# Performance work log

Measured on AMD Instinct MI355X. Metric: run time of the kernel, lower is better.

The kernel has to match this reference:

```python
import jax, jax.numpy as jnp
import numpy as np

B, T, H = 32, 1024, 1024


def setup_inputs() -> dict:
    key = jax.random.key(0)
    k1, k2, k3, k4, k5 = jax.random.split(key, 5)
    h_t = jax.random.normal(k1, (B, H), dtype=jnp.float32)
    enc_out = jax.random.normal(k2, (B, T, H), dtype=jnp.float32)
    src_mask = jnp.ones((B, T), dtype=bool)
    s = 1.0 / np.sqrt(H)
    Wa = jax.random.normal(k3, (H, H), dtype=jnp.float32) * s
    Ua = jax.random.normal(k4, (H, H), dtype=jnp.float32) * s
    va = jax.random.normal(k5, (H,), dtype=jnp.float32) * s
    return {"h_t": h_t, "enc_out": enc_out, "src_mask": src_mask,
            "Wa": Wa, "Ua": Ua, "va": va}


def reference(h_t, enc_out, src_mask, Wa, Ua, va):
    # h_proj: [B,H] ; enc_proj: [B,T,H]
    h_proj = h_t @ Wa.T
    enc_proj = jnp.einsum('bth,kh->btk', enc_out, Ua)
    # additive score: va . tanh(Wa h + Ua enc)  -> [B,T]
    e = jnp.einsum('bth,h->bt', jnp.tanh(h_proj[:, None, :] + enc_proj), va)
    e = jnp.where(src_mask, e, -jnp.inf)
    attn = jax.nn.softmax(e, axis=1)                     # [B,T]
    context = jnp.einsum('bt,bth->bh', attn, enc_out)    # [B,H]
    return context, attn
```

## Files before the change

kernel.cpp:

```cpp
#include <hip/hip_runtime.h>

#define BB 32
#define TT 1024
#define HH 1024
#define MM (BB * TT)

typedef __bf16 bf16x8 __attribute__((ext_vector_type(8)));
typedef float  f32x4  __attribute__((ext_vector_type(4)));

__device__ __forceinline__ void async_copy16(const void* g, void* l) {
  __builtin_amdgcn_global_load_lds(
      (const __attribute__((address_space(1))) void*)g,
      (__attribute__((address_space(3))) void*)l, 16, 0, 0);
}

__device__ __forceinline__ float fast_tanh(float x) {
  float e2 = __expf(2.f * x);
  return 1.f - 2.f * __builtin_amdgcn_rcpf(e2 + 1.f);
}

#define NCHUNK_ENC 4194304
#define CVT_BLKS   2112
#define CVT_STRIDE (CVT_BLKS * 256)
__global__ __launch_bounds__(256) void prep_kernel(
    const float* __restrict__ enc, const float* __restrict__ Ua,
    const float* __restrict__ h_t, const float* __restrict__ Wa,
    __bf16* __restrict__ encb, __bf16* __restrict__ uab,
    float* __restrict__ hp, float* __restrict__ e) {
  const int blk = blockIdx.x;
  const int tid = threadIdx.x;

  if (blk < CVT_BLKS) {
    int F = blk * 256 + tid;
#pragma unroll
    for (int it = 0; it < 8; ++it, F += CVT_STRIDE) {
      const float* src;
      __bf16* dst;
      int R;
      if (F < NCHUNK_ENC) { src = enc; dst = encb; R = F; }
      else                { src = Ua;  dst = uab;  R = F - NCHUNK_ENC; }
      const int c   = R & 2047;
      const int t   = R >> 11;
      const int kt  = t & 15;
      const int rt  = t >> 4;
      const int u   = c >> 10;
      const int idx = (c >> 3) & 127;
      const int s   = c & 7;
      const int g   = s ^ (idx & 7);
      const int row = (idx & 63) + ((idx >> 6) & 1) * 128 + u * 64;
      const float* sp = src + (((size_t)rt * 256 + row) << 10) + (kt << 6) + (g << 3);
      f32x4 a  = *(const f32x4*)sp;
      f32x4 b2 = *(const f32x4*)(sp + 4);
      bf16x8 o;
      o[0] = (__bf16)a[0];  o[1] = (__bf16)a[1];
      o[2] = (__bf16)a[2];  o[3] = (__bf16)a[3];
      o[4] = (__bf16)b2[0]; o[5] = (__bf16)b2[1];
      o[6] = (__bf16)b2[2]; o[7] = (__bf16)b2[3];
      *(bf16x8*)(dst + (size_t)R * 8) = o;
    }
  } else if (blk < 2240) {
    const int hb = blk - CVT_BLKS;
    const int b  = hb >> 2;
    const int k  = (hb & 3) * 256 + tid;
    __shared__ float hs[HH];
    for (int i = tid; i < HH; i += 256) hs[i] = h_t[b * HH + i];
    __syncthreads();
    const float4* w  = (const float4*)(Wa + (size_t)k * HH);
    const float4* hv = (const float4*)hs;
    float acc = 0.f;
#pragma unroll 8
    for (int i = 0; i < HH / 4; ++i) {
      float4 a = w[i];
      float4 h = hv[i];
      acc += a.x * h.x + a.y * h.y + a.z * h.z + a.w * h.w;
    }
    hp[b * HH + k] = acc;
  } else {
    f32x4 z = {0.f, 0.f, 0.f, 0.f};
    f32x4* ep = (f32x4*)e;
#pragma unroll
    for (int i = 0; i < 32; ++i) ep[i * 256 + tid] = z;
  }
}

__global__ __launch_bounds__(128) void hproj_kernel(
    const float* __restrict__ h_t, const float* __restrict__ Wa,
    float* __restrict__ hp) {
  const int k = blockIdx.x * 128 + threadIdx.x;
  const int b = blockIdx.y;
  __shared__ float hs[HH];
  for (int i = threadIdx.x; i < HH; i += 128) hs[i] = h_t[b * HH + i];
  __syncthreads();
  const float4* w  = (const float4*)(Wa + (size_t)k * HH);
  const float4* hv = (const float4*)hs;
  float acc = 0.f;
#pragma unroll 8
  for (int i = 0; i < HH / 4; ++i) {
    float4 a = w[i];
    float4 h = hv[i];
    acc += a.x * h.x + a.y * h.y + a.z * h.z + a.w * h.w;
  }
  hp[b * HH + k] = acc;
}

__global__ __launch_bounds__(512, 2) void score_8ph_kernel(
    const __bf16* __restrict__ encb, const __bf16* __restrict__ uab,
    const float* __restrict__ hp, const float* __restrict__ va,
    float* __restrict__ e) {
  __shared__ __bf16 As[2][16384];
  __shared__ __bf16 Bs[2][16384];

  const int wg = blockIdx.x;
  const int sw = (wg & 7) * 64 + (wg >> 3);
  const int nt = sw & 3;
  const int mt = sw >> 2;
  const int b  = mt >> 2;

  const int tid  = threadIdx.x;
  const int lane = tid & 63;
  const int wid  = tid >> 6;
  const int wr   = wid >> 2;
  const int wc   = wid & 3;
  const int rl   = lane & 15;
  const int kq   = lane >> 4;
  const int e7   = rl & 7;

  const __bf16* Ag = encb + ((size_t)(mt * 16) << 14);
  const __bf16* Bg = uab  + ((size_t)(nt * 16) << 14);

  const int s0 = ((kq ^ e7) << 4);
  const int s1 = (((kq + 4) ^ e7) << 4);
  const int arow = (rl + wr * 64) * 128;
  const int brow = (rl + (wc >> 1) * 64) * 128 + (wc & 1) * 16384;

#define LDA(buf, mi, sl) (*(const bf16x8*)((const char*)(buf) + \
    (((mi) >> 2) * 16384 + ((mi) & 3) * 2048) + arow + (sl)))
#define LDB(buf, nj, sl) (*(const bf16x8*)((const char*)(buf) + \
    ((nj) * 2048) + brow + (sl)))

#define STAGE(gb, kt2, lp, u) do { \
    const __bf16* _g = (gb) + (((size_t)(kt2)) << 14) + (((u) << 10) + tid) * 8; \
    __bf16* _l = (lp) + (((u) << 10) + tid) * 8; \
    async_copy16(_g, _l); \
    async_copy16(_g + 4096, _l + 4096); \
  } while (0)

#define MFMA16(ml, kkb) do { \
    _Pragma("unroll") \
    for (int nj = 0; nj < 4; ++nj) { \
      acc[(ml) + 0][nj] = __builtin_amdgcn_mfma_f32_16x16x32_bf16(af0, bfr[(kkb) + nj], acc[(ml) + 0][nj], 0, 0, 0); \
      acc[(ml) + 1][nj] = __builtin_amdgcn_mfma_f32_16x16x32_bf16(af1, bfr[(kkb) + nj], acc[(ml) + 1][nj], 0, 0, 0); \
      acc[(ml) + 2][nj] = __builtin_amdgcn_mfma_f32_16x16x32_bf16(af2, bfr[(kkb) + nj], acc[(ml) + 2][nj], 0, 0, 0); \
      acc[(ml) + 3][nj] = __builtin_amdgcn_mfma_f32_16x16x32_bf16(af3, bfr[(kkb) + nj], acc[(ml) + 3][nj], 0, 0, 0); \
    } \
  } while (0)

  f32x4 acc[8][4] = {};
  bf16x8 bfr[8];

  STAGE(Ag, 0, &As[0][0], 0);
  STAGE(Bg, 0, &Bs[0][0], 0);
  STAGE(Bg, 0, &Bs[0][0], 1);
  STAGE(Ag, 0, &As[0][0], 1);
  STAGE(Bg, 1, &Bs[1][0], 0);
  STAGE(Bg, 1, &Bs[1][0], 1);
  STAGE(Ag, 1, &As[1][0], 0);
  asm volatile("s_waitcnt vmcnt(6)" ::: "memory");
  __builtin_amdgcn_s_barrier();

  for (int t = 0; t < 15; ++t) {
    const int p = t & 1;
    const char* Ab = (const char*)&As[p][0];
    const char* Bb = (const char*)&Bs[p][0];

    {
#pragma unroll
      for (int nj = 0; nj < 4; ++nj) { bfr[nj] = LDB(Bb, nj, s0); bfr[4 + nj] = LDB(Bb, nj, s1); }
      bf16x8 af0 = LDA(Ab, 0, s0), af1 = LDA(Ab, 1, s0), af2 = LDA(Ab, 2, s0), af3 = LDA(Ab, 3, s0);
      STAGE(Ag, t + 1, &As[p ^ 1][0], 1);
      __builtin_amdgcn_s_barrier();
      asm volatile("s_waitcnt lgkmcnt(0)" ::: "memory");
      __builtin_amdgcn_s_setprio(1);
      MFMA16(0, 0);
      __builtin_amdgcn_s_setprio(0);
      __builtin_amdgcn_s_barrier();
    }
    {
      bf16x8 af0 = LDA(Ab, 0, s1), af1 = LDA(Ab, 1, s1), af2 = LDA(Ab, 2, s1), af3 = LDA(Ab, 3, s1);
      if (t < 14) STAGE(Bg, t + 2, &Bs[p][0], 0);
      __builtin_amdgcn_s_barrier();
      asm volatile("s_waitcnt lgkmcnt(0)" ::: "memory");
      __builtin_amdgcn_s_setprio(1);
      MFMA16(0, 4);
      __builtin_amdgcn_s_setprio(0);
      __builtin_amdgcn_s_barrier();
    }
    {
      bf16x8 af0 = LDA(Ab, 4, s0), af1 = LDA(Ab, 5, s0), af2 = LDA(Ab, 6, s0), af3 = LDA(Ab, 7, s0);
      if (t < 14) STAGE(Bg, t + 2, &Bs[p][0], 1);
      __builtin_amdgcn_s_barrier();
      asm volatile("s_waitcnt lgkmcnt(0)" ::: "memory");
      __builtin_amdgcn_s_setprio(1);
      MFMA16(4, 0);
      __builtin_amdgcn_s_setprio(0);
      __builtin_amdgcn_s_barrier();
    }
    {
      bf16x8 af0 = LDA(Ab, 4, s1), af1 = LDA(Ab, 5, s1), af2 = LDA(Ab, 6, s1), af3 = LDA(Ab, 7, s1);
      if (t < 14) STAGE(Ag, t + 2, &As[p][0], 0);
      __builtin_amdgcn_s_barrier();
      asm volatile("s_waitcnt lgkmcnt(0)" ::: "memory");
      __builtin_amdgcn_s_setprio(1);
      MFMA16(4, 4);
      __builtin_amdgcn_s_setprio(0);
      if (t < 14) asm volatile("s_waitcnt vmcnt(6)" ::: "memory");
      else        asm volatile("s_waitcnt vmcnt(0)" ::: "memory");
      __builtin_amdgcn_s_barrier();
    }
  }

  {
    const char* Ab = (const char*)&As[1][0];
    const char* Bb = (const char*)&Bs[1][0];
    {
#pragma unroll
      for (int nj = 0; nj < 4; ++nj) { bfr[nj] = LDB(Bb, nj, s0); bfr[4 + nj] = LDB(Bb, nj, s1); }
      bf16x8 af0 = LDA(Ab, 0, s0), af1 = LDA(Ab, 1, s0), af2 = LDA(Ab, 2, s0), af3 = LDA(Ab, 3, s0);
      __builtin_amdgcn_s_barrier();
      asm volatile("s_waitcnt lgkmcnt(0)" ::: "memory");
      __builtin_amdgcn_s_setprio(1);
      MFMA16(0, 0);
      __builtin_amdgcn_s_setprio(0);
      __builtin_amdgcn_s_barrier();
    }
    {
      bf16x8 af0 = LDA(Ab, 0, s1), af1 = LDA(Ab, 1, s1), af2 = LDA(Ab, 2, s1), af3 = LDA(Ab, 3, s1);
      __builtin_amdgcn_s_barrier();
      asm volatile("s_waitcnt lgkmcnt(0)" ::: "memory");
      __builtin_amdgcn_s_setprio(1);
      MFMA16(0, 4);
      __builtin_amdgcn_s_setprio(0);
      __builtin_amdgcn_s_barrier();
    }
    {
      bf16x8 af0 = LDA(Ab, 4, s0), af1 = LDA(Ab, 5, s0), af2 = LDA(Ab, 6, s0), af3 = LDA(Ab, 7, s0);
      __builtin_amdgcn_s_barrier();
      asm volatile("s_waitcnt lgkmcnt(0)" ::: "memory");
      __builtin_amdgcn_s_setprio(1);
      MFMA16(4, 0);
      __builtin_amdgcn_s_setprio(0);
      __builtin_amdgcn_s_barrier();
    }
    {
      bf16x8 af0 = LDA(Ab, 4, s1), af1 = LDA(Ab, 5, s1), af2 = LDA(Ab, 6, s1), af3 = LDA(Ab, 7, s1);
      __builtin_amdgcn_s_barrier();
      asm volatile("s_waitcnt lgkmcnt(0)" ::: "memory");
      __builtin_amdgcn_s_setprio(1);
      MFMA16(4, 4);
      __builtin_amdgcn_s_setprio(0);
    }
  }

  const float* hpb = hp + (b << 10);
#pragma unroll
  for (int mi = 0; mi < 8; ++mi) {
    float rs[4] = {0.f, 0.f, 0.f, 0.f};
#pragma unroll
    for (int nj = 0; nj < 4; ++nj) {
      const int col  = nt * 256 + wc * 64 + nj * 16 + rl;
      const float hv = hpb[col];
      const float vv = va[col];
#pragma unroll
      for (int j = 0; j < 4; ++j)
        rs[j] += fast_tanh(acc[mi][nj][j] + hv) * vv;
    }
#pragma unroll
    for (int j = 0; j < 4; ++j) {
      float r = rs[j];
      r += __shfl_xor(r, 1);
      r += __shfl_xor(r, 2);
      r += __shfl_xor(r, 4);
      r += __shfl_xor(r, 8);
      if (rl == 0)
        atomicAdd(&e[mt * 256 + wr * 128 + mi * 16 + kq * 4 + j], r);
    }
  }
#undef LDA
#undef LDB
#undef STAGE
#undef MFMA16
}

#define BM 128
#define BN 128
#define BK 32

__device__ __forceinline__ bf16x8 cvt8(const float* p) {
  f32x4 a = *(const f32x4*)p;
  f32x4 b = *(const f32x4*)(p + 4);
  bf16x8 r;
  r[0] = (__bf16)a[0]; r[1] = (__bf16)a[1]; r[2] = (__bf16)a[2]; r[3] = (__bf16)a[3];
  r[4] = (__bf16)b[0]; r[5] = (__bf16)b[1]; r[6] = (__bf16)b[2]; r[7] = (__bf16)b[3];
  return r;
}

__device__ __forceinline__ void score_epilogue(
    f32x4 acc[4][4], int m0, int n0, int b, int lane, int wr, int wc,
    const float* __restrict__ hp, const float* __restrict__ va,
    float* __restrict__ e) {
  const int rl = lane & 15;
  const int rq = lane >> 4;
#pragma unroll
  for (int mi = 0; mi < 4; ++mi) {
    float rs[4] = {0.f, 0.f, 0.f, 0.f};
#pragma unroll
    for (int nj = 0; nj < 4; ++nj) {
      const int col  = n0 + wc * 64 + nj * 16 + rl;
      const float hv = hp[(b << 10) + col];
      const float vv = va[col];
#pragma unroll
      for (int j = 0; j < 4; ++j)
        rs[j] += fast_tanh(acc[mi][nj][j] + hv) * vv;
    }
#pragma unroll
    for (int j = 0; j < 4; ++j) {
      float r = rs[j];
      r += __shfl_xor(r, 1);
      r += __shfl_xor(r, 2);
      r += __shfl_xor(r, 4);
      r += __shfl_xor(r, 8);
      if (rl == 0)
        atomicAdd(&e[m0 + wr * 64 + mi * 16 + rq * 4 + j], r);
    }
  }
}

__global__ __launch_bounds__(256) void score_f32_kernel(
    const float* __restrict__ enc, const float* __restrict__ Ua,
    const float* __restrict__ hp, const float* __restrict__ va,
    float* __restrict__ e) {
  const int m0 = blockIdx.x * BM;
  const int n0 = blockIdx.y * BN;
  const int b  = m0 >> 10;

  __shared__ float As[BM * BK];
  __shared__ float Bs[BN * BK];

  const int tid  = threadIdx.x;
  const int lane = tid & 63;
  const int wid  = tid >> 6;
  const int wr   = wid >> 1;
  const int wc   = wid & 1;

  f32x4 acc[4][4] = {};

  const int srow = tid >> 3;
  const int scol = (tid & 7) * 4;
  const float* gA = enc + (((size_t)(m0 + srow)) << 10) + scol;
  const float* gB = Ua  + (((size_t)(n0 + srow)) << 10) + scol;
  float* lA = As + srow * BK + scol;
  float* lB = Bs + srow * BK + scol;

  for (int kt = 0; kt < HH / BK; ++kt) {
    const int h0 = kt * BK;
    __syncthreads();
#pragma unroll
    for (int i = 0; i < 4; ++i) {
      async_copy16(gA + ((size_t)(i * 32) << 10) + h0, lA + i * 32 * BK);
      async_copy16(gB + ((size_t)(i * 32) << 10) + h0, lB + i * 32 * BK);
    }
    __syncthreads();

    const int koff = (lane >> 4) * 8;
    const int rl   = lane & 15;
    bf16x8 af[4], bfr[4];
#pragma unroll
    for (int mi = 0; mi < 4; ++mi)
      af[mi] = cvt8(As + (wr * 64 + mi * 16 + rl) * BK + koff);
#pragma unroll
    for (int nj = 0; nj < 4; ++nj)
      bfr[nj] = cvt8(Bs + (wc * 64 + nj * 16 + rl) * BK + koff);
#pragma unroll
    for (int mi = 0; mi < 4; ++mi)
#pragma unroll
      for (int nj = 0; nj < 4; ++nj)
        acc[mi][nj] = __builtin_amdgcn_mfma_f32_16x16x32_bf16(
            af[mi], bfr[nj], acc[mi][nj], 0, 0, 0);
  }

  score_epilogue(acc, m0, n0, b, lane, wr, wc, hp, va, e);
}

__global__ __launch_bounds__(256) void softmax_kernel(
    const float* __restrict__ e, const int* __restrict__ mask,
    float* __restrict__ attn) {
  const int b   = blockIdx.x;
  const int tid = threadIdx.x;
  const float* eb = e + (b << 10);
  const int*   mb = mask + (b << 10);
  float v[4];
  float mx = -INFINITY;
#pragma unroll
  for (int j = 0; j < 4; ++j) {
    const int t = tid + j * 256;
    float x = mb[t] ? eb[t] : -INFINITY;
    v[j] = x;
    mx = fmaxf(mx, x);
  }
#pragma unroll
  for (int s = 1; s < 64; s <<= 1) mx = fmaxf(mx, __shfl_xor(mx, s));
  __shared__ float redm[4];
  if ((tid & 63) == 0) redm[tid >> 6] = mx;
  __syncthreads();
  mx = fmaxf(fmaxf(redm[0], redm[1]), fmaxf(redm[2], redm[3]));

  float s = 0.f;
#pragma unroll
  for (int j = 0; j < 4; ++j) { v[j] = __expf(v[j] - mx); s += v[j]; }
#pragma unroll
  for (int st = 1; st < 64; st <<= 1) s += __shfl_xor(s, st);
  __shared__ float reds[4];
  if ((tid & 63) == 0) reds[tid >> 6] = s;
  __syncthreads();
  s = reds[0] + reds[1] + reds[2] + reds[3];
  const float inv = 1.f / s;
#pragma unroll
  for (int j = 0; j < 4; ++j) attn[(b << 10) + tid + j * 256] = v[j] * inv;
}

__global__ __launch_bounds__(256) void context2_kernel(
    const __bf16* __restrict__ encb, const float* __restrict__ attn,
    float* __restrict__ ctx) {
  const int q   = blockIdx.x;
  const int b   = blockIdx.y;
  const int tid = threadIdx.x;
  const int h8l = tid & 15;
  const int tq  = tid >> 4;
  const int h8g = q * 16 + h8l;
  const int kt  = h8g >> 3;
  const int g   = h8g & 7;

  __shared__ float at[1024];
  for (int i = tid; i < 1024; i += 256) at[i] = attn[(b << 10) + i];
  __syncthreads();

  const int rt = b * 4 + (tq >> 2);
  const int u  = tq & 1;
  const int b7 = (tq >> 1) & 1;
  const __bf16* base = encb + (((size_t)(rt * 16 + kt)) << 14)
                       + (u << 13) + (b7 << 12);
  const float* ap = at + tq * 64;

  float acc[8] = {};
#pragma unroll 8
  for (int j = 0; j < 64; ++j) {
    bf16x8 v = *(const bf16x8*)(base + j * 64 + ((g ^ (j & 7)) << 3));
    const float w = ap[j];
#pragma unroll
    for (int ee = 0; ee < 8; ++ee) acc[ee] += w * (float)v[ee];
  }

  __shared__ float red[16][16][8];
#pragma unroll
  for (int ee = 0; ee < 8; ++ee) red[tq][h8l][ee] = acc[ee];
  __syncthreads();

  if (tid < 128) {
    const int h8 = tid >> 3;
    const int ee = tid & 7;
    float s = 0.f;
#pragma unroll
    for (int r = 0; r < 16; ++r) s += red[r][h8][ee];
    ctx[(b << 10) + q * 128 + h8 * 8 + ee] = s;
  }
}

__global__ __launch_bounds__(256) void context_kernel(
    const float* __restrict__ attn, const float* __restrict__ enc,
    float* __restrict__ ctx) {
  const int h  = blockIdx.x * 256 + threadIdx.x;
  const int b  = blockIdx.y;
  const int t0 = blockIdx.z * 128;
  const float* ab = attn + (b << 10) + t0;
  const float* eb = enc + (((size_t)(b << 10) + t0) << 10) + h;
  float acc = 0.f;
#pragma unroll 4
  for (int t = 0; t < 128; ++t)
    acc = fmaf(ab[t], eb[(size_t)t << 10], acc);
  atomicAdd(&ctx[(b << 10) + h], acc);
}

extern "C" void kernel_launch(void* const* d_in, const int* in_sizes, int n_in,
                              void* d_out, int out_size, void* d_ws, size_t ws_size,
                              hipStream_t stream) {
  const float* h_t  = (const float*)d_in[0];
  const float* enc  = (const float*)d_in[1];
  const int*   mask = (const int*)d_in[2];
  const float* Wa   = (const float*)d_in[3];
  const float* Ua   = (const float*)d_in[4];
  const float* va   = (const float*)d_in[5];

  float* out = (float*)d_out;
  float* e   = (float*)d_ws;
  float* hp  = e + MM;

  const size_t base   = 2 * (size_t)MM * sizeof(float);
  const size_t encb_n = (size_t)MM * HH;
  const size_t uab_n  = (size_t)HH * HH;
  const size_t need   = base + (encb_n + uab_n) * sizeof(__bf16);

  if (ws_size >= need) {
    __bf16* encb = (__bf16*)((char*)d_ws + base);
    __bf16* uab  = encb + encb_n;
    prep_kernel<<<2241, 256, 0, stream>>>(enc, Ua, h_t, Wa, encb, uab, hp, e);
    score_8ph_kernel<<<512, 512, 0, stream>>>(encb, uab, hp, va, e);
    softmax_kernel<<<BB, 256, 0, stream>>>(e, mask, out + BB * HH);
    context2_kernel<<<dim3(8, BB), 256, 0, stream>>>(encb, out + BB * HH, out);
  } else {
    hipMemsetAsync(e, 0, MM * sizeof(float), stream);
    hipMemsetAsync(out, 0, BB * HH * sizeof(float), stream);
    hproj_kernel<<<dim3(HH / 128, BB), 128, 0, stream>>>(h_t, Wa, hp);
    score_f32_kernel<<<dim3(MM / BM, HH / BN), 256, 0, stream>>>(enc, Ua, hp, va, e);
    softmax_kernel<<<BB, 256, 0, stream>>>(e, mask, out + BB * HH);
    context_kernel<<<dim3(HH / 256, BB, 8), 256, 0, stream>>>(out + BB * HH, enc, out);
  }
}
```

Before: 156.9 us.

## Fuse enc fp32-to-bf16 conversion into score GEMM A-tile loading

Drops the separate pass that converted the whole encoder tensor to a swizzled bf16 copy. The score kernel now loads fp32 A tiles from global into registers, converts them, and writes bf16 into shared memory inside the pipelined loop. Ua conversion moves into a small prep kernel, and the context kernel reads fp32 enc directly. This removes a 128MB read plus 64MB write round trip. In exchange the GEMM uses more registers (occupancy hint lowered to 1), does synchronous register-staged loads instead of async LDS copies, and the context pass reads twice the bytes.

```diff
diff --git a/kernel.cpp b/kernel.cpp
--- a/kernel.cpp
+++ b/kernel.cpp
@@ -19,49 +19,16 @@
   return 1.f - 2.f * __builtin_amdgcn_rcpf(e2 + 1.f);
 }
 
-#define NCHUNK_ENC 4194304
-#define CVT_BLKS   2112
-#define CVT_STRIDE (CVT_BLKS * 256)
-__global__ __launch_bounds__(256) void prep_kernel(
-    const float* __restrict__ enc, const float* __restrict__ Ua,
-    const float* __restrict__ h_t, const float* __restrict__ Wa,
-    __bf16* __restrict__ encb, __bf16* __restrict__ uab,
+__global__ __launch_bounds__(256) void mini_prep_kernel(
+    const float* __restrict__ Ua, const float* __restrict__ h_t,
+    const float* __restrict__ Wa, __bf16* __restrict__ uab,
     float* __restrict__ hp, float* __restrict__ e) {
   const int blk = blockIdx.x;
   const int tid = threadIdx.x;
 
-  if (blk < CVT_BLKS) {
-    int F = blk * 256 + tid;
-#pragma unroll
-    for (int it = 0; it < 8; ++it, F += CVT_STRIDE) {
-      const float* src;
-      __bf16* dst;
-      int R;
-      if (F < NCHUNK_ENC) { src = enc; dst = encb; R = F; }
-      else                { src = Ua;  dst = uab;  R = F - NCHUNK_ENC; }
-      const int c   = R & 2047;
-      const int t   = R >> 11;
-      const int kt  = t & 15;
-      const int rt  = t >> 4;
-      const int u   = c >> 10;
-      const int idx = (c >> 3) & 127;
-      const int s   = c & 7;
-      const int g   = s ^ (idx & 7);
-      const int row = (idx & 63) + ((idx >> 6) & 1) * 128 + u * 64;
-      const float* sp = src + (((size_t)rt * 256 + row) << 10) + (kt << 6) + (g << 3);
-      f32x4 a  = *(const f32x4*)sp;
-      f32x4 b2 = *(const f32x4*)(sp + 4);
-      bf16x8 o;
-      o[0] = (__bf16)a[0];  o[1] = (__bf16)a[1];
-      o[2] = (__bf16)a[2];  o[3] = (__bf16)a[3];
-      o[4] = (__bf16)b2[0]; o[5] = (__bf16)b2[1];
-      o[6] = (__bf16)b2[2]; o[7] = (__bf16)b2[3];
-      *(bf16x8*)(dst + (size_t)R * 8) = o;
-    }
-  } else if (blk < 2240) {
-    const int hb = blk - CVT_BLKS;
-    const int b  = hb >> 2;
-    const int k  = (hb & 3) * 256 + tid;
+  if (blk < 128) {
+    const int b = blk >> 2;
+    const int k = (blk & 3) * 256 + tid;
     __shared__ float hs[HH];
     for (int i = tid; i < HH; i += 256) hs[i] = h_t[b * HH + i];
     __syncthreads();
@@ -75,6 +42,29 @@
       acc += a.x * h.x + a.y * h.y + a.z * h.z + a.w * h.w;
     }
     hp[b * HH + k] = acc;
+  } else if (blk < 256) {
+    int F = (blk - 128) * 256 + tid;
+#pragma unroll
+    for (int it = 0; it < 4; ++it, F += 32768) {
+      const int c   = F & 2047;
+      const int t   = F >> 11;
+      const int kt  = t & 15;
+      const int rt  = t >> 4;
+      const int u   = c >> 10;
+      const int idx = (c >> 3) & 127;
+      const int s   = c & 7;
+      const int g   = s ^ (idx & 7);
+      const int row = (idx & 63) + ((idx >> 6) & 1) * 128 + u * 64;
+      const float* sp = Ua + (((size_t)rt * 256 + row) << 10) + (kt << 6) + (g << 3);
+      f32x4 a  = *(const f32x4*)sp;
+      f32x4 b2 = *(const f32x4*)(sp + 4);
+      bf16x8 o;
+      o[0] = (__bf16)a[0];  o[1] = (__bf16)a[1];
+      o[2] = (__bf16)a[2];  o[3] = (__bf16)a[3];
+      o[4] = (__bf16)b2[0]; o[5] = (__bf16)b2[1];
+      o[6] = (__bf16)b2[2]; o[7] = (__bf16)b2[3];
+      *(bf16x8*)(uab + (size_t)F * 8) = o;
+    }
   } else {
     f32x4 z = {0.f, 0.f, 0.f, 0.f};
     f32x4* ep = (f32x4*)e;
@@ -103,8 +93,8 @@
   hp[b * HH + k] = acc;
 }
 
-__global__ __launch_bounds__(512, 2) void score_8ph_kernel(
-    const __bf16* __restrict__ encb, const __bf16* __restrict__ uab,
+__global__ __launch_bounds__(512, 1) void score_8ph_kernel(
+    const float* __restrict__ enc, const __bf16* __restrict__ uab,
     const float* __restrict__ hp, const float* __restrict__ va,
     float* __restrict__ e) {
   __shared__ __bf16 As[2][16384];
@@ -125,8 +115,11 @@
   const int kq   = lane >> 4;
   const int e7   = rl & 7;
 
-  const __bf16* Ag = encb + ((size_t)(mt * 16) << 14);
-  const __bf16* Bg = uab  + ((size_t)(nt * 16) << 14);
+  const float* Af = enc + ((size_t)(mt * 256) << 10);
+  const __bf16* Bg = uab + ((size_t)(nt * 16) << 14);
+
+  const int aidx = tid >> 3;
+  const int ag8  = ((tid & 7) ^ (aidx & 7)) << 3;
 
   const int s0 = ((kq ^ e7) << 4);
   const int s1 = (((kq + 4) ^ e7) << 4);
@@ -138,11 +131,33 @@
 #define LDB(buf, nj, sl) (*(const bf16x8*)((const char*)(buf) + \
     ((nj) * 2048) + brow + (sl)))
 
-#define STAGE(gb, kt2, lp, u) do { \
-    const __bf16* _g = (gb) + (((size_t)(kt2)) << 14) + (((u) << 10) + tid) * 8; \
+#define BSTAGE(kt2, lp, u) do { \
+    const __bf16* _g = Bg + (((size_t)(kt2)) << 14) + (((u) << 10) + tid) * 8; \
     __bf16* _l = (lp) + (((u) << 10) + tid) * 8; \
     async_copy16(_g, _l); \
     async_copy16(_g + 4096, _l + 4096); \
+  } while (0)
+
+#define ALOAD(ra, rb, rc, rd, kt2, u) do { \
+    const float* _p1 = Af + ((size_t)(aidx + (u) * 64) << 10) + ((kt2) << 6) + ag8; \
+    const float* _p2 = _p1 + (128 << 10); \
+    ra = *(const f32x4*)_p1; rb = *(const f32x4*)(_p1 + 4); \
+    rc = *(const f32x4*)_p2; rd = *(const f32x4*)(_p2 + 4); \
+  } while (0)
+
+#define AWRITE(lp, u, ra, rb, rc, rd) do { \
+    __bf16* _l = (lp) + ((u) << 13) + tid * 8; \
+    bf16x8 o1, o2; \
+    o1[0] = (__bf16)ra[0]; o1[1] = (__bf16)ra[1]; \
+    o1[2] = (__bf16)ra[2]; o1[3] = (__bf16)ra[3]; \
+    o1[4] = (__bf16)rb[0]; o1[5] = (__bf16)rb[1]; \
+    o1[6] = (__bf16)rb[2]; o1[7] = (__bf16)rb[3]; \
+    o2[0] = (__bf16)rc[0]; o2[1] = (__bf16)rc[1]; \
+    o2[2] = (__bf16)rc[2]; o2[3] = (__bf16)rc[3]; \
+    o2[4] = (__bf16)rd[0]; o2[5] = (__bf16)rd[1]; \
+    o2[6] = (__bf16)rd[2]; o2[7] = (__bf16)rd[3]; \
+    *(bf16x8*)_l = o1; \
+    *(bf16x8*)(_l + 4096) = o2; \
   } while (0)
 
 #define MFMA16(ml, kkb) do { \
@@ -157,27 +172,33 @@
 
   f32x4 acc[8][4] = {};
   bf16x8 bfr[8];
-
-  STAGE(Ag, 0, &As[0][0], 0);
-  STAGE(Bg, 0, &Bs[0][0], 0);
-  STAGE(Bg, 0, &Bs[0][0], 1);
-  STAGE(Ag, 0, &As[0][0], 1);
-  STAGE(Bg, 1, &Bs[1][0], 0);
-  STAGE(Bg, 1, &Bs[1][0], 1);
-  STAGE(Ag, 1, &As[1][0], 0);
-  asm volatile("s_waitcnt vmcnt(6)" ::: "memory");
+  f32x4 xa, xb, xc, xd;
+  f32x4 ya, yb, yc, yd;
+
+  ALOAD(xa, xb, xc, xd, 0, 0);
+  BSTAGE(0, &Bs[0][0], 0);
+  BSTAGE(0, &Bs[0][0], 1);
+  ALOAD(ya, yb, yc, yd, 0, 1);
+  BSTAGE(1, &Bs[1][0], 0);
+  BSTAGE(1, &Bs[1][0], 1);
+  asm volatile("s_waitcnt vmcnt(4)" ::: "memory");
+  AWRITE(&As[0][0], 0, xa, xb, xc, xd);
+  AWRITE(&As[0][0], 1, ya, yb, yc, yd);
+  ALOAD(xa, xb, xc, xd, 1, 0);
+  asm volatile("s_waitcnt lgkmcnt(0)" ::: "memory");
   __builtin_amdgcn_s_barrier();
 
   for (int t = 0; t < 15; ++t) {
     const int p = t & 1;
     const char* Ab = (const char*)&As[p][0];
     const char* Bb = (const char*)&Bs[p][0];
+    __bf16* An = &As[p ^ 1][0];
 
     {
 #pragma unroll
       for (int nj = 0; nj < 4; ++nj) { bfr[nj] = LDB(Bb, nj, s0); bfr[4 + nj] = LDB(Bb, nj, s1); }
       bf16x8 af0 = LDA(Ab, 0, s0), af1 = LDA(Ab, 1, s0), af2 = LDA(Ab, 2, s0), af3 = LDA(Ab, 3, s0);
-      STAGE(Ag, t + 1, &As[p ^ 1][0], 1);
+      ALOAD(ya, yb, yc, yd, t + 1, 1);
       __builtin_amdgcn_s_barrier();
       asm volatile("s_waitcnt lgkmcnt(0)" ::: "memory");
       __builtin_amdgcn_s_setprio(1);
@@ -187,7 +208,7 @@
     }
     {
       bf16x8 af0 = LDA(Ab, 0, s1), af1 = LDA(Ab, 1, s1), af2 = LDA(Ab, 2, s1), af3 = LDA(Ab, 3, s1);
-      if (t < 14) STAGE(Bg, t + 2, &Bs[p][0], 0);
+      if (t < 14) BSTAGE(t + 2, &Bs[p][0], 0);
       __builtin_amdgcn_s_barrier();
       asm volatile("s_waitcnt lgkmcnt(0)" ::: "memory");
       __builtin_amdgcn_s_setprio(1);
@@ -197,7 +218,7 @@
     }
     {
       bf16x8 af0 = LDA(Ab, 4, s0), af1 = LDA(Ab, 5, s0), af2 = LDA(Ab, 6, s0), af3 = LDA(Ab, 7, s0);
-      if (t < 14) STAGE(Bg, t + 2, &Bs[p][0], 1);
+      if (t < 14) BSTAGE(t + 2, &Bs[p][0], 1);
       __builtin_amdgcn_s_barrier();
       asm volatile("s_waitcnt lgkmcnt(0)" ::: "memory");
       __builtin_amdgcn_s_setprio(1);
@@ -207,14 +228,17 @@
     }
     {
       bf16x8 af0 = LDA(Ab, 4, s1), af1 = LDA(Ab, 5, s1), af2 = LDA(Ab, 6, s1), af3 = LDA(Ab, 7, s1);
-      if (t < 14) STAGE(Ag, t + 2, &As[p][0], 0);
       __builtin_amdgcn_s_barrier();
       asm volatile("s_waitcnt lgkmcnt(0)" ::: "memory");
       __builtin_amdgcn_s_setprio(1);
       MFMA16(4, 4);
       __builtin_amdgcn_s_setprio(0);
-      if (t < 14) asm volatile("s_waitcnt vmcnt(6)" ::: "memory");
+      if (t < 14) asm volatile("s_waitcnt vmcnt(4)" ::: "memory");
       else        asm volatile("s_waitcnt vmcnt(0)" ::: "memory");
+      AWRITE(An, 0, xa, xb, xc, xd);
+      AWRITE(An, 1, ya, yb, yc, yd);
+      if (t < 14) ALOAD(xa, xb, xc, xd, t + 2, 0);
+      asm volatile("s_waitcnt lgkmcnt(0)" ::: "memory");
       __builtin_amdgcn_s_barrier();
     }
   }
@@ -287,7 +311,9 @@
   }
 #undef LDA
 #undef LDB
-#undef STAGE
+#undef BSTAGE
+#undef ALOAD
+#undef AWRITE
 #undef MFMA16
 }
 
@@ -428,50 +454,43 @@
   for (int j = 0; j < 4; ++j) attn[(b << 10) + tid + j * 256] = v[j] * inv;
 }
 
-__global__ __launch_bounds__(256) void context2_kernel(
-    const __bf16* __restrict__ encb, const float* __restrict__ attn,
+__global__ __launch_bounds__(256) void context_f32_kernel(
+    const float* __restrict__ enc, const float* __restrict__ attn,
     float* __restrict__ ctx) {
   const int q   = blockIdx.x;
   const int b   = blockIdx.y;
   const int tid = threadIdx.x;
-  const int h8l = tid & 15;
-  const int tq  = tid >> 4;
-  const int h8g = q * 16 + h8l;
-  const int kt  = h8g >> 3;
-  const int g   = h8g & 7;
+  const int h4  = tid & 31;
+  const int tg  = tid >> 5;
 
   __shared__ float at[1024];
   for (int i = tid; i < 1024; i += 256) at[i] = attn[(b << 10) + i];
   __syncthreads();
 
-  const int rt = b * 4 + (tq >> 2);
-  const int u  = tq & 1;
-  const int b7 = (tq >> 1) & 1;
-  const __bf16* base = encb + (((size_t)(rt * 16 + kt)) << 14)
-                       + (u << 13) + (b7 << 12);
-  const float* ap = at + tq * 64;
-
-  float acc[8] = {};
-#pragma unroll 8
-  for (int j = 0; j < 64; ++j) {
-    bf16x8 v = *(const bf16x8*)(base + j * 64 + ((g ^ (j & 7)) << 3));
-    const float w = ap[j];
-#pragma unroll
-    for (int ee = 0; ee < 8; ++ee) acc[ee] += w * (float)v[ee];
-  }
-
-  __shared__ float red[16][16][8];
-#pragma unroll
-  for (int ee = 0; ee < 8; ++ee) red[tq][h8l][ee] = acc[ee];
+  const float* ebase = enc + ((size_t)b << 20) + ((size_t)(tg * 128) << 10)
+                       + q * 128 + h4 * 4;
+  const float* ap = at + tg * 128;
+  f32x4 acc = {0.f, 0.f, 0.f, 0.f};
+#pragma unroll 4
+  for (int t = 0; t < 128; ++t) {
+    f32x4 v = *(const f32x4*)(ebase + ((size_t)t << 10));
+    const float w = ap[t];
+    acc[0] += w * v[0]; acc[1] += w * v[1];
+    acc[2] += w * v[2]; acc[3] += w * v[3];
+  }
+
+  __shared__ f32x4 red[8][32];
+  red[tg][h4] = acc;
   __syncthreads();
 
-  if (tid < 128) {
-    const int h8 = tid >> 3;
-    const int ee = tid & 7;
-    float s = 0.f;
-#pragma unroll
-    for (int r = 0; r < 16; ++r) s += red[r][h8][ee];
-    ctx[(b << 10) + q * 128 + h8 * 8 + ee] = s;
+  if (tid < 32) {
+    f32x4 s = red[0][tid];
+#pragma unroll
+    for (int r = 1; r < 8; ++r) {
+      f32x4 v = red[r][tid];
+      s[0] += v[0]; s[1] += v[1]; s[2] += v[2]; s[3] += v[3];
+    }
+    *(f32x4*)(ctx + (b << 10) + q * 128 + tid * 4) = s;
   }
 }
 
@@ -504,18 +523,16 @@
   float* e   = (float*)d_ws;
   float* hp  = e + MM;
 
-  const size_t base   = 2 * (size_t)MM * sizeof(float);
-  const size_t encb_n = (size_t)MM * HH;
-  const size_t uab_n  = (size_t)HH * HH;
-  const size_t need   = base + (encb_n + uab_n) * sizeof(__bf16);
+  const size_t base  = 2 * (size_t)MM * sizeof(float);
+  const size_t uab_n = (size_t)HH * HH;
+  const size_t need  = base + uab_n * sizeof(__bf16);
 
   if (ws_size >= need) {
-    __bf16* encb = (__bf16*)((char*)d_ws + base);
-    __bf16* uab  = encb + encb_n;
-    prep_kernel<<<2241, 256, 0, stream>>>(enc, Ua, h_t, Wa, encb, uab, hp, e);
-    score_8ph_kernel<<<512, 512, 0, stream>>>(encb, uab, hp, va, e);
+    __bf16* uab = (__bf16*)((char*)d_ws + base);
+    mini_prep_kernel<<<257, 256, 0, stream>>>(Ua, h_t, Wa, uab, hp, e);
+    score_8ph_kernel<<<512, 512, 0, stream>>>(enc, uab, hp, va, e);
     softmax_kernel<<<BB, 256, 0, stream>>>(e, mask, out + BB * HH);
-    context2_kernel<<<dim3(8, BB), 256, 0, stream>>>(encb, out + BB * HH, out);
+    context_f32_kernel<<<dim3(8, BB), 256, 0, stream>>>(enc, out + BB * HH, out);
   } else {
     hipMemsetAsync(e, 0, MM * sizeof(float), stream);
     hipMemsetAsync(out, 0, BB * HH * sizeof(float), stream);
```

Result: faster. 137.7 us (-12.2%).
